# Performance work log

Hardware: AMD Instinct MI355X
Metric: run time of the kernel (lower is better)

The kernel has to match this reference:

```python
import jax, jax.numpy as jnp
import numpy as np

BS, NS, S = 4, 16384, 8
C_PLANE, RES = 64, 128
IN_DIM = 3 * C_PLANE  # 192


def _bilerp(plane, uv):
    """plane: [B,C,H,W]; uv: [B,n,2] in [0,1] -> [B,n,C] bilinear samples (border clamp)."""
    B, C, H, W = plane.shape
    x = jnp.clip(uv[..., 0], 0.0, 1.0) * (W - 1)
    y = jnp.clip(uv[..., 1], 0.0, 1.0) * (H - 1)
    x0 = jnp.floor(x).astype(jnp.int32)
    y0 = jnp.floor(y).astype(jnp.int32)
    x1 = jnp.minimum(x0 + 1, W - 1)
    y1 = jnp.minimum(y0 + 1, H - 1)
    wx = (x - x0)[:, :, None]
    wy = (y - y0)[:, :, None]
    gat = jax.vmap(lambda p, yy, xx: p[:, yy, xx].T)  # per-batch gather -> [n,C]
    f00 = gat(plane, y0, x0)
    f01 = gat(plane, y0, x1)
    f10 = gat(plane, y1, x0)
    f11 = gat(plane, y1, x1)
    return (f00 * (1 - wx) * (1 - wy) + f01 * wx * (1 - wy)
            + f10 * (1 - wx) * wy + f11 * wx * wy)


def _sample_triplane(p, feat_xz, feat_xy, feat_yz):
    """p: [B,n,3] -> concat of bilinear samples from the three planes: [B,n,3C]."""
    f_xz = _bilerp(feat_xz, p[..., jnp.array([0, 2])])
    f_xy = _bilerp(feat_xy, p[..., jnp.array([0, 1])])
    f_yz = _bilerp(feat_yz, p[..., jnp.array([1, 2])])
    return jnp.concatenate([f_xz, f_xy, f_yz], axis=-1)


def setup_inputs() -> dict:
    key = jax.random.key(0)
    ks = jax.random.split(key, 12)
    w = 0.05  # small init so predicted offsets stay near the query point
    return {
        "query_pos": jax.random.uniform(ks[0], (BS, NS, 3), dtype=jnp.float32),
        "feat_xz": jax.random.normal(ks[1], (BS, C_PLANE, RES, RES), dtype=jnp.float32),
        "feat_xy": jax.random.normal(ks[2], (BS, C_PLANE, RES, RES), dtype=jnp.float32),
        "feat_yz": jax.random.normal(ks[3], (BS, C_PLANE, RES, RES), dtype=jnp.float32),
        "W_v": jax.random.normal(ks[4], (IN_DIM, IN_DIM), dtype=jnp.float32) * w,
        "b_v": jnp.zeros((IN_DIM,), jnp.float32),
        "W_out": jax.random.normal(ks[5], (IN_DIM, IN_DIM), dtype=jnp.float32) * w,
        "b_out": jnp.zeros((IN_DIM,), jnp.float32),
        "W_off": jax.random.normal(ks[6], (3 * S, IN_DIM), dtype=jnp.float32) * w,
        "b_off": jnp.zeros((3 * S,), jnp.float32),
        "W_wt": jax.random.normal(ks[7], (S, IN_DIM), dtype=jnp.float32) * w,
        "b_wt": jnp.zeros((S,), jnp.float32),
    }


def reference(query_pos, feat_xz, feat_xy, feat_yz, W_v, b_v, W_out, b_out,
              W_off, b_off, W_wt, b_wt):
    bs, ns, _ = query_pos.shape
    # feature at query points: [bs, ns, IN_DIM]
    feature = _sample_triplane(query_pos, feat_xz, feat_xy, feat_yz)
    # predicted per-sample offsets and weights
    off = (feature @ W_off.T + b_off).reshape(bs, ns, S, 3)
    wt = (feature @ W_wt.T + b_wt)[..., None]            # [bs, ns, S, 1]
    pts = off + query_pos[:, :, None, :]                  # [bs, ns, S, 3]
    # gather features at offset locations: [bs, ns*S, IN_DIM]
    aux = _sample_triplane(pts.reshape(bs, ns * S, 3), feat_xz, feat_xy, feat_yz)
    v = (aux @ W_v.T + b_v).reshape(bs, ns, S, -1)        # [bs, ns, S, hidden]
    out = (v * wt).sum(axis=-2)                           # weighted sum over samples
    out = out @ W_out.T + b_out + feature                 # residual add
    return out  # [bs, ns, IN_DIM]
```

## Files before the change

kernel.cpp:

```cpp
#include <hip/hip_runtime.h>

#define BS 4
#define NS 16384
#define S_SAMP 8
#define CPL 64
#define RES 128
#define IN_DIM 192
#define NPTS (BS * NS)
#define PL_STRIDE (RES * RES * CPL)
#define PLANES_T_FLOATS (BS * 3 * PL_STRIDE)

__global__ __launch_bounds__(256) void transpose_planes(
    const float* __restrict__ xz, const float* __restrict__ xy,
    const float* __restrict__ yz, float* __restrict__ T) {
  __shared__ float tile[64][33];
  int blk = blockIdx.x;
  int xt = blk & 3;
  int y  = (blk >> 2) & 127;
  int pl = (blk >> 9) % 3;
  int b  = blk / 1536;
  const float* src = (pl == 0) ? xz : ((pl == 1) ? xy : yz);
  src += (size_t)b * CPL * RES * RES + (size_t)y * RES + xt * 32;
  int tid = threadIdx.x;
  int xl = tid & 31, c0 = tid >> 5;
#pragma unroll
  for (int r = 0; r < 8; ++r) {
    int c = c0 + (r << 3);
    tile[c][xl] = src[(size_t)c * RES * RES + xl];
  }
  __syncthreads();
  float* dst = T + ((size_t)(b * 3 + pl) * RES * RES + (size_t)y * RES + xt * 32) * CPL;
  int c2 = tid & 63, x0 = tid >> 6;
#pragma unroll
  for (int r = 0; r < 8; ++r) {
    int xl2 = x0 + (r << 2);
    dst[(size_t)xl2 * CPL + c2] = tile[c2][xl2];
  }
}

__global__ __launch_bounds__(192) void precompute_wc(
    const float* __restrict__ W_v, const float* __restrict__ b_v,
    const float* __restrict__ W_out, float* __restrict__ WcT,
    float* __restrict__ bc) {
  int j = blockIdx.x;
  int k = threadIdx.x;
  if (j < IN_DIM) {
    float acc = 0.f;
    for (int m = 0; m < IN_DIM; ++m)
      acc += W_out[j * IN_DIM + m] * W_v[m * IN_DIM + k];
    WcT[k * IN_DIM + j] = acc;
  } else {
    float acc = 0.f;
    for (int m = 0; m < IN_DIM; ++m)
      acc += W_out[k * IN_DIM + m] * b_v[m];
    bc[k] = acc;
  }
}

__device__ __forceinline__ void mkaddr(const float* __restrict__ pb, float u,
                                       float v, const float*& b00, int& dx,
                                       int& dy, float& wx, float& wy) {
  u = fminf(fmaxf(u, 0.f), 1.f) * 127.f;
  v = fminf(fmaxf(v, 0.f), 1.f) * 127.f;
  float xf = floorf(u), yf = floorf(v);
  wx = u - xf;
  wy = v - yf;
  int x0 = __builtin_amdgcn_readfirstlane((int)xf);
  int y0 = __builtin_amdgcn_readfirstlane((int)yf);
  dx = (x0 < 127) ? CPL : 0;
  dy = (y0 < 127) ? RES * CPL : 0;
  b00 = pb + (((y0 << 7) + x0) << 6);
}

__global__ __launch_bounds__(256, 4) void fused_sample(
    const float* __restrict__ qpos, const float* __restrict__ planesT,
    const float* __restrict__ W_off, const float* __restrict__ b_off,
    const float* __restrict__ W_wt, const float* __restrict__ b_wt,
    float* __restrict__ waux, float* __restrict__ swtg,
    float* __restrict__ featg) {
  __shared__ float feat_lds[8][IN_DIM];
  __shared__ float offwt[8][32];
  int w = threadIdx.x >> 6, lane = threadIdx.x & 63;
  int p0 = blockIdx.x * 8 + w * 2;
  int p1 = p0 + 1;
  int b0 = p0 >> 14, b1 = p1 >> 14;
  float qx0 = qpos[p0 * 3 + 0], qy0 = qpos[p0 * 3 + 1], qz0 = qpos[p0 * 3 + 2];
  float qx1 = qpos[p1 * 3 + 0], qy1 = qpos[p1 * 3 + 1], qz1 = qpos[p1 * 3 + 2];
  const float* Tb0 = planesT + (size_t)b0 * 3 * PL_STRIDE;
  const float* Tb1 = planesT + (size_t)b1 * 3 * PL_STRIDE;

  float f[6];
  {
    const float* B[6]; int DX[6], DY[6]; float WX[6], WY[6];
    mkaddr(Tb0,                 qx0, qz0, B[0], DX[0], DY[0], WX[0], WY[0]);
    mkaddr(Tb0 + PL_STRIDE,     qx0, qy0, B[1], DX[1], DY[1], WX[1], WY[1]);
    mkaddr(Tb0 + 2 * PL_STRIDE, qy0, qz0, B[2], DX[2], DY[2], WX[2], WY[2]);
    mkaddr(Tb1,                 qx1, qz1, B[3], DX[3], DY[3], WX[3], WY[3]);
    mkaddr(Tb1 + PL_STRIDE,     qx1, qy1, B[4], DX[4], DY[4], WX[4], WY[4]);
    mkaddr(Tb1 + 2 * PL_STRIDE, qy1, qz1, B[5], DX[5], DY[5], WX[5], WY[5]);
    float t00[6], t01[6], t10[6], t11[6];
#pragma unroll
    for (int i = 0; i < 6; ++i) {
      t00[i] = B[i][lane];
      t01[i] = B[i][DX[i] + lane];
      t10[i] = B[i][DY[i] + lane];
      t11[i] = B[i][DY[i] + DX[i] + lane];
    }
#pragma unroll
    for (int i = 0; i < 6; ++i) {
      float a = t00[i] + WX[i] * (t01[i] - t00[i]);
      float c = t10[i] + WX[i] * (t11[i] - t10[i]);
      f[i] = a + WY[i] * (c - a);
    }
  }
  feat_lds[w * 2 + 0][lane] = f[0];
  feat_lds[w * 2 + 0][64 + lane] = f[1];
  feat_lds[w * 2 + 0][128 + lane] = f[2];
  feat_lds[w * 2 + 1][lane] = f[3];
  feat_lds[w * 2 + 1][64 + lane] = f[4];
  feat_lds[w * 2 + 1][128 + lane] = f[5];
  __syncthreads();

  {
    int pt = lane >> 5, oj = lane & 31;
    const float* row = (oj < 24) ? (W_off + oj * IN_DIM)
                                 : (W_wt + (oj - 24) * IN_DIM);
    float bias = (oj < 24) ? b_off[oj] : b_wt[oj - 24];
    const float4* r4 = (const float4*)row;
    const float4* fl = (const float4*)feat_lds[w * 2 + pt];
    float a0 = 0.f, a1 = 0.f, a2 = 0.f, a3 = 0.f;
#pragma unroll
    for (int k4 = 0; k4 < IN_DIM / 4; ++k4) {
      float4 rv = r4[k4];
      float4 fv = fl[k4];
      a0 += rv.x * fv.x;
      a1 += rv.y * fv.y;
      a2 += rv.z * fv.z;
      a3 += rv.w * fv.w;
    }
    offwt[w * 2 + pt][oj] = bias + ((a0 + a1) + (a2 + a3));
  }
  __syncthreads();

  float wa[2][3] = {};
  float swt0 = 0.f, swt1 = 0.f;
#pragma unroll 2
  for (int s = 0; s < S_SAMP; ++s) {
    float ox0 = offwt[w * 2 + 0][3 * s + 0];
    float oy0 = offwt[w * 2 + 0][3 * s + 1];
    float oz0 = offwt[w * 2 + 0][3 * s + 2];
    float wt0 = offwt[w * 2 + 0][24 + s];
    float ox1 = offwt[w * 2 + 1][3 * s + 0];
    float oy1 = offwt[w * 2 + 1][3 * s + 1];
    float oz1 = offwt[w * 2 + 1][3 * s + 2];
    float wt1 = offwt[w * 2 + 1][24 + s];
    float px0 = qx0 + ox0, py0 = qy0 + oy0, pz0 = qz0 + oz0;
    float px1 = qx1 + ox1, py1 = qy1 + oy1, pz1 = qz1 + oz1;

    const float* B[6]; int DX[6], DY[6]; float WX[6], WY[6];
    mkaddr(Tb0,                 px0, pz0, B[0], DX[0], DY[0], WX[0], WY[0]);
    mkaddr(Tb0 + PL_STRIDE,     px0, py0, B[1], DX[1], DY[1], WX[1], WY[1]);
    mkaddr(Tb0 + 2 * PL_STRIDE, py0, pz0, B[2], DX[2], DY[2], WX[2], WY[2]);
    mkaddr(Tb1,                 px1, pz1, B[3], DX[3], DY[3], WX[3], WY[3]);
    mkaddr(Tb1 + PL_STRIDE,     px1, py1, B[4], DX[4], DY[4], WX[4], WY[4]);
    mkaddr(Tb1 + 2 * PL_STRIDE, py1, pz1, B[5], DX[5], DY[5], WX[5], WY[5]);
    float t00[6], t01[6], t10[6], t11[6];
#pragma unroll
    for (int i = 0; i < 6; ++i) {
      t00[i] = B[i][lane];
      t01[i] = B[i][DX[i] + lane];
      t10[i] = B[i][DY[i] + lane];
      t11[i] = B[i][DY[i] + DX[i] + lane];
    }
    float r[6];
#pragma unroll
    for (int i = 0; i < 6; ++i) {
      float a = t00[i] + WX[i] * (t01[i] - t00[i]);
      float c = t10[i] + WX[i] * (t11[i] - t10[i]);
      r[i] = a + WY[i] * (c - a);
    }
    wa[0][0] += wt0 * r[0]; wa[0][1] += wt0 * r[1]; wa[0][2] += wt0 * r[2];
    wa[1][0] += wt1 * r[3]; wa[1][1] += wt1 * r[4]; wa[1][2] += wt1 * r[5];
    swt0 += wt0; swt1 += wt1;
  }

  size_t o0 = (size_t)p0 * IN_DIM + lane;
  size_t o1 = (size_t)p1 * IN_DIM + lane;
  waux[o0] = wa[0][0]; waux[o0 + 64] = wa[0][1]; waux[o0 + 128] = wa[0][2];
  waux[o1] = wa[1][0]; waux[o1 + 64] = wa[1][1]; waux[o1 + 128] = wa[1][2];
  if (lane == 0) { swtg[p0] = swt0; swtg[p1] = swt1; }
  featg[o0] = f[0]; featg[o0 + 64] = f[1]; featg[o0 + 128] = f[2];
  featg[o1] = f[3]; featg[o1 + 64] = f[4]; featg[o1 + 128] = f[5];
}

__global__ __launch_bounds__(256) void out_gemm(
    const float* __restrict__ waux, const float* __restrict__ swtg,
    const float* __restrict__ WcT, const float* __restrict__ bc,
    const float* __restrict__ b_out, float* __restrict__ out) {
  __shared__ float at[64 * IN_DIM];
  int tid = threadIdx.x;
  int w = tid >> 6, lane = tid & 63;
  int p0 = blockIdx.x * 64;

  const float4* src = (const float4*)(waux + (size_t)p0 * IN_DIM);
  float4* dst4 = (float4*)at;
#pragma unroll
  for (int i = 0; i < 12; ++i) dst4[tid + i * 256] = src[tid + i * 256];
  __syncthreads();

  int pw = w * 16;
  float acc[16][3] = {};
  for (int c = 0; c < 3; ++c) {
    const float* wc = WcT + c * 64 * IN_DIM;
#pragma unroll 2
    for (int k4 = 0; k4 < 16; ++k4) {
      float v0[4], v1[4], v2[4];
#pragma unroll
      for (int kk = 0; kk < 4; ++kk) {
        const float* r = wc + (k4 * 4 + kk) * IN_DIM;
        v0[kk] = r[lane];
        v1[kk] = r[64 + lane];
        v2[kk] = r[128 + lane];
      }
#pragma unroll
      for (int q = 0; q < 16; ++q) {
        float4 a4 = *(const float4*)&at[(pw + q) * IN_DIM + c * 64 + k4 * 4];
        acc[q][0] += v0[0] * a4.x + v0[1] * a4.y + v0[2] * a4.z + v0[3] * a4.w;
        acc[q][1] += v1[0] * a4.x + v1[1] * a4.y + v1[2] * a4.z + v1[3] * a4.w;
        acc[q][2] += v2[0] * a4.x + v2[1] * a4.y + v2[2] * a4.z + v2[3] * a4.w;
      }
    }
  }

  float bcv[3], bov[3];
#pragma unroll
  for (int t = 0; t < 3; ++t) {
    bcv[t] = bc[lane + t * 64];
    bov[t] = b_out[lane + t * 64];
  }
#pragma unroll
  for (int q = 0; q < 16; ++q) {
    int p = p0 + pw + q;
    float sw = swtg[p];
#pragma unroll
    for (int t = 0; t < 3; ++t) {
      size_t o = (size_t)p * IN_DIM + lane + t * 64;
      out[o] = acc[q][t] + sw * bcv[t] + bov[t] + out[o];
    }
  }
}

extern "C" void kernel_launch(void* const* d_in, const int* in_sizes, int n_in,
                              void* d_out, int out_size, void* d_ws,
                              size_t ws_size, hipStream_t stream) {
  const float* qpos  = (const float*)d_in[0];
  const float* xz    = (const float*)d_in[1];
  const float* xy    = (const float*)d_in[2];
  const float* yz    = (const float*)d_in[3];
  const float* W_v   = (const float*)d_in[4];
  const float* b_v   = (const float*)d_in[5];
  const float* W_out = (const float*)d_in[6];
  const float* b_out = (const float*)d_in[7];
  const float* W_off = (const float*)d_in[8];
  const float* b_off = (const float*)d_in[9];
  const float* W_wt  = (const float*)d_in[10];
  const float* b_wt  = (const float*)d_in[11];

  float* ws      = (float*)d_ws;
  float* planesT = ws;
  float* waux    = planesT + PLANES_T_FLOATS;
  float* swtg    = waux + (size_t)NPTS * IN_DIM;
  float* WcT     = swtg + NPTS;
  float* bc      = WcT + IN_DIM * IN_DIM;
  float* out     = (float*)d_out;

  hipLaunchKernelGGL(transpose_planes, dim3(BS * 3 * RES * 4), dim3(256), 0,
                     stream, xz, xy, yz, planesT);
  hipLaunchKernelGGL(precompute_wc, dim3(IN_DIM + 1), dim3(IN_DIM), 0, stream,
                     W_v, b_v, W_out, WcT, bc);
  hipLaunchKernelGGL(fused_sample, dim3(NPTS / 8), dim3(256), 0, stream, qpos,
                     planesT, W_off, b_off, W_wt, b_wt, waux, swtg, out);
  hipLaunchKernelGGL(out_gemm, dim3(NPTS / 64), dim3(256), 0, stream, waux,
                     swtg, WcT, bc, b_out, out);
}
```

Before: 482.2 us.

## Software-pipeline sample tap loads and shrink out_gemm tile to 32 points

The sample loop in fused_sample now uses double-buffered tap registers, issuing the gathers for sample s+1 before interpolating sample s so memory latency overlaps arithmetic. out_gemm processes 32 points per block instead of 64, with a single flattened k loop and batched LDS reads, which halves LDS use and doubles the grid. Holding two tap sets raises register pressure and may reduce occupancy. The smaller GEMM tile reloads the weights from global memory twice as often.

```diff
diff --git a/kernel.cpp b/kernel.cpp
--- a/kernel.cpp
+++ b/kernel.cpp
@@ -72,6 +72,55 @@
   b00 = pb + (((y0 << 7) + x0) << 6);
 }
 
+struct Taps {
+  float t00[6], t01[6], t10[6], t11[6];
+  float wx[6], wy[6];
+  float wt0, wt1;
+};
+
+__device__ __forceinline__ void load_taps(
+    int s, const float* __restrict__ ow0, const float* __restrict__ ow1,
+    float qx0, float qy0, float qz0, float qx1, float qy1, float qz1,
+    const float* __restrict__ Tb0, const float* __restrict__ Tb1, int lane,
+    Taps& T) {
+  float px0 = qx0 + ow0[3 * s + 0];
+  float py0 = qy0 + ow0[3 * s + 1];
+  float pz0 = qz0 + ow0[3 * s + 2];
+  T.wt0 = ow0[24 + s];
+  float px1 = qx1 + ow1[3 * s + 0];
+  float py1 = qy1 + ow1[3 * s + 1];
+  float pz1 = qz1 + ow1[3 * s + 2];
+  T.wt1 = ow1[24 + s];
+  const float* B[6];
+  int DX[6], DY[6];
+  mkaddr(Tb0,                 px0, pz0, B[0], DX[0], DY[0], T.wx[0], T.wy[0]);
+  mkaddr(Tb0 + PL_STRIDE,     px0, py0, B[1], DX[1], DY[1], T.wx[1], T.wy[1]);
+  mkaddr(Tb0 + 2 * PL_STRIDE, py0, pz0, B[2], DX[2], DY[2], T.wx[2], T.wy[2]);
+  mkaddr(Tb1,                 px1, pz1, B[3], DX[3], DY[3], T.wx[3], T.wy[3]);
+  mkaddr(Tb1 + PL_STRIDE,     px1, py1, B[4], DX[4], DY[4], T.wx[4], T.wy[4]);
+  mkaddr(Tb1 + 2 * PL_STRIDE, py1, pz1, B[5], DX[5], DY[5], T.wx[5], T.wy[5]);
+#pragma unroll
+  for (int i = 0; i < 6; ++i) {
+    T.t00[i] = B[i][lane];
+    T.t01[i] = B[i][DX[i] + lane];
+    T.t10[i] = B[i][DY[i] + lane];
+    T.t11[i] = B[i][DY[i] + DX[i] + lane];
+  }
+}
+
+__device__ __forceinline__ void lerp_acc(const Taps& T, float wa[6],
+                                         float& swt0, float& swt1) {
+#pragma unroll
+  for (int i = 0; i < 6; ++i) {
+    float a = T.t00[i] + T.wx[i] * (T.t01[i] - T.t00[i]);
+    float c = T.t10[i] + T.wx[i] * (T.t11[i] - T.t10[i]);
+    float r = a + T.wy[i] * (c - a);
+    wa[i] += ((i < 3) ? T.wt0 : T.wt1) * r;
+  }
+  swt0 += T.wt0;
+  swt1 += T.wt1;
+}
+
 __global__ __launch_bounds__(256, 4) void fused_sample(
     const float* __restrict__ qpos, const float* __restrict__ planesT,
     const float* __restrict__ W_off, const float* __restrict__ b_off,
@@ -81,7 +130,8 @@
   __shared__ float feat_lds[8][IN_DIM];
   __shared__ float offwt[8][32];
   int w = threadIdx.x >> 6, lane = threadIdx.x & 63;
-  int p0 = blockIdx.x * 8 + w * 2;
+  int w2 = w * 2;
+  int p0 = blockIdx.x * 8 + w2;
   int p1 = p0 + 1;
   int b0 = p0 >> 14, b1 = p1 >> 14;
   float qx0 = qpos[p0 * 3 + 0], qy0 = qpos[p0 * 3 + 1], qz0 = qpos[p0 * 3 + 2];
@@ -113,12 +163,12 @@
       f[i] = a + WY[i] * (c - a);
     }
   }
-  feat_lds[w * 2 + 0][lane] = f[0];
-  feat_lds[w * 2 + 0][64 + lane] = f[1];
-  feat_lds[w * 2 + 0][128 + lane] = f[2];
-  feat_lds[w * 2 + 1][lane] = f[3];
-  feat_lds[w * 2 + 1][64 + lane] = f[4];
-  feat_lds[w * 2 + 1][128 + lane] = f[5];
+  feat_lds[w2 + 0][lane] = f[0];
+  feat_lds[w2 + 0][64 + lane] = f[1];
+  feat_lds[w2 + 0][128 + lane] = f[2];
+  feat_lds[w2 + 1][lane] = f[3];
+  feat_lds[w2 + 1][64 + lane] = f[4];
+  feat_lds[w2 + 1][128 + lane] = f[5];
   __syncthreads();
 
   {
@@ -127,7 +177,7 @@
                                  : (W_wt + (oj - 24) * IN_DIM);
     float bias = (oj < 24) ? b_off[oj] : b_wt[oj - 24];
     const float4* r4 = (const float4*)row;
-    const float4* fl = (const float4*)feat_lds[w * 2 + pt];
+    const float4* fl = (const float4*)feat_lds[w2 + pt];
     float a0 = 0.f, a1 = 0.f, a2 = 0.f, a3 = 0.f;
 #pragma unroll
     for (int k4 = 0; k4 < IN_DIM / 4; ++k4) {
@@ -138,56 +188,30 @@
       a2 += rv.z * fv.z;
       a3 += rv.w * fv.w;
     }
-    offwt[w * 2 + pt][oj] = bias + ((a0 + a1) + (a2 + a3));
+    offwt[w2 + pt][oj] = bias + ((a0 + a1) + (a2 + a3));
   }
   __syncthreads();
 
-  float wa[2][3] = {};
+  const float* ow0 = offwt[w2 + 0];
+  const float* ow1 = offwt[w2 + 1];
+  float wa[6] = {};
   float swt0 = 0.f, swt1 = 0.f;
-#pragma unroll 2
-  for (int s = 0; s < S_SAMP; ++s) {
-    float ox0 = offwt[w * 2 + 0][3 * s + 0];
-    float oy0 = offwt[w * 2 + 0][3 * s + 1];
-    float oz0 = offwt[w * 2 + 0][3 * s + 2];
-    float wt0 = offwt[w * 2 + 0][24 + s];
-    float ox1 = offwt[w * 2 + 1][3 * s + 0];
-    float oy1 = offwt[w * 2 + 1][3 * s + 1];
-    float oz1 = offwt[w * 2 + 1][3 * s + 2];
-    float wt1 = offwt[w * 2 + 1][24 + s];
-    float px0 = qx0 + ox0, py0 = qy0 + oy0, pz0 = qz0 + oz0;
-    float px1 = qx1 + ox1, py1 = qy1 + oy1, pz1 = qz1 + oz1;
-
-    const float* B[6]; int DX[6], DY[6]; float WX[6], WY[6];
-    mkaddr(Tb0,                 px0, pz0, B[0], DX[0], DY[0], WX[0], WY[0]);
-    mkaddr(Tb0 + PL_STRIDE,     px0, py0, B[1], DX[1], DY[1], WX[1], WY[1]);
-    mkaddr(Tb0 + 2 * PL_STRIDE, py0, pz0, B[2], DX[2], DY[2], WX[2], WY[2]);
-    mkaddr(Tb1,                 px1, pz1, B[3], DX[3], DY[3], WX[3], WY[3]);
-    mkaddr(Tb1 + PL_STRIDE,     px1, py1, B[4], DX[4], DY[4], WX[4], WY[4]);
-    mkaddr(Tb1 + 2 * PL_STRIDE, py1, pz1, B[5], DX[5], DY[5], WX[5], WY[5]);
-    float t00[6], t01[6], t10[6], t11[6];
-#pragma unroll
-    for (int i = 0; i < 6; ++i) {
-      t00[i] = B[i][lane];
-      t01[i] = B[i][DX[i] + lane];
-      t10[i] = B[i][DY[i] + lane];
-      t11[i] = B[i][DY[i] + DX[i] + lane];
-    }
-    float r[6];
-#pragma unroll
-    for (int i = 0; i < 6; ++i) {
-      float a = t00[i] + WX[i] * (t01[i] - t00[i]);
-      float c = t10[i] + WX[i] * (t11[i] - t10[i]);
-      r[i] = a + WY[i] * (c - a);
-    }
-    wa[0][0] += wt0 * r[0]; wa[0][1] += wt0 * r[1]; wa[0][2] += wt0 * r[2];
-    wa[1][0] += wt1 * r[3]; wa[1][1] += wt1 * r[4]; wa[1][2] += wt1 * r[5];
-    swt0 += wt0; swt1 += wt1;
+  Taps TA, TB;
+  load_taps(0, ow0, ow1, qx0, qy0, qz0, qx1, qy1, qz1, Tb0, Tb1, lane, TA);
+#pragma unroll
+  for (int s = 0; s < S_SAMP; s += 2) {
+    if (s + 1 < S_SAMP)
+      load_taps(s + 1, ow0, ow1, qx0, qy0, qz0, qx1, qy1, qz1, Tb0, Tb1, lane, TB);
+    lerp_acc(TA, wa, swt0, swt1);
+    if (s + 2 < S_SAMP)
+      load_taps(s + 2, ow0, ow1, qx0, qy0, qz0, qx1, qy1, qz1, Tb0, Tb1, lane, TA);
+    lerp_acc(TB, wa, swt0, swt1);
   }
 
   size_t o0 = (size_t)p0 * IN_DIM + lane;
   size_t o1 = (size_t)p1 * IN_DIM + lane;
-  waux[o0] = wa[0][0]; waux[o0 + 64] = wa[0][1]; waux[o0 + 128] = wa[0][2];
-  waux[o1] = wa[1][0]; waux[o1 + 64] = wa[1][1]; waux[o1 + 128] = wa[1][2];
+  waux[o0] = wa[0]; waux[o0 + 64] = wa[1]; waux[o0 + 128] = wa[2];
+  waux[o1] = wa[3]; waux[o1 + 64] = wa[4]; waux[o1 + 128] = wa[5];
   if (lane == 0) { swtg[p0] = swt0; swtg[p1] = swt1; }
   featg[o0] = f[0]; featg[o0 + 64] = f[1]; featg[o0 + 128] = f[2];
   featg[o1] = f[3]; featg[o1 + 64] = f[4]; featg[o1 + 128] = f[5];
@@ -197,38 +221,38 @@
     const float* __restrict__ waux, const float* __restrict__ swtg,
     const float* __restrict__ WcT, const float* __restrict__ bc,
     const float* __restrict__ b_out, float* __restrict__ out) {
-  __shared__ float at[64 * IN_DIM];
+  __shared__ float at[32 * IN_DIM];
   int tid = threadIdx.x;
   int w = tid >> 6, lane = tid & 63;
-  int p0 = blockIdx.x * 64;
+  int p0 = blockIdx.x * 32;
 
   const float4* src = (const float4*)(waux + (size_t)p0 * IN_DIM);
   float4* dst4 = (float4*)at;
 #pragma unroll
-  for (int i = 0; i < 12; ++i) dst4[tid + i * 256] = src[tid + i * 256];
+  for (int i = 0; i < 6; ++i) dst4[tid + i * 256] = src[tid + i * 256];
   __syncthreads();
 
-  int pw = w * 16;
-  float acc[16][3] = {};
-  for (int c = 0; c < 3; ++c) {
-    const float* wc = WcT + c * 64 * IN_DIM;
+  int pw = w * 8;
+  float acc[8][3] = {};
 #pragma unroll 2
-    for (int k4 = 0; k4 < 16; ++k4) {
-      float v0[4], v1[4], v2[4];
-#pragma unroll
-      for (int kk = 0; kk < 4; ++kk) {
-        const float* r = wc + (k4 * 4 + kk) * IN_DIM;
-        v0[kk] = r[lane];
-        v1[kk] = r[64 + lane];
-        v2[kk] = r[128 + lane];
-      }
-#pragma unroll
-      for (int q = 0; q < 16; ++q) {
-        float4 a4 = *(const float4*)&at[(pw + q) * IN_DIM + c * 64 + k4 * 4];
-        acc[q][0] += v0[0] * a4.x + v0[1] * a4.y + v0[2] * a4.z + v0[3] * a4.w;
-        acc[q][1] += v1[0] * a4.x + v1[1] * a4.y + v1[2] * a4.z + v1[3] * a4.w;
-        acc[q][2] += v2[0] * a4.x + v2[1] * a4.y + v2[2] * a4.z + v2[3] * a4.w;
-      }
+  for (int k4 = 0; k4 < 48; ++k4) {
+    float v0[4], v1[4], v2[4];
+#pragma unroll
+    for (int kk = 0; kk < 4; ++kk) {
+      const float* r = WcT + (k4 * 4 + kk) * IN_DIM;
+      v0[kk] = r[lane];
+      v1[kk] = r[64 + lane];
+      v2[kk] = r[128 + lane];
+    }
+    float4 a[8];
+#pragma unroll
+    for (int q = 0; q < 8; ++q)
+      a[q] = *(const float4*)&at[(pw + q) * IN_DIM + k4 * 4];
+#pragma unroll
+    for (int q = 0; q < 8; ++q) {
+      acc[q][0] += v0[0] * a[q].x + v0[1] * a[q].y + v0[2] * a[q].z + v0[3] * a[q].w;
+      acc[q][1] += v1[0] * a[q].x + v1[1] * a[q].y + v1[2] * a[q].z + v1[3] * a[q].w;
+      acc[q][2] += v2[0] * a[q].x + v2[1] * a[q].y + v2[2] * a[q].z + v2[3] * a[q].w;
     }
   }
 
@@ -239,7 +263,7 @@
     bov[t] = b_out[lane + t * 64];
   }
 #pragma unroll
-  for (int q = 0; q < 16; ++q) {
+  for (int q = 0; q < 8; ++q) {
     int p = p0 + pw + q;
     float sw = swtg[p];
 #pragma unroll
@@ -280,6 +304,6 @@
                      W_v, b_v, W_out, WcT, bc);
   hipLaunchKernelGGL(fused_sample, dim3(NPTS / 8), dim3(256), 0, stream, qpos,
                      planesT, W_off, b_off, W_wt, b_wt, waux, swtg, out);
-  hipLaunchKernelGGL(out_gemm, dim3(NPTS / 64), dim3(256), 0, stream, waux,
+  hipLaunchKernelGGL(out_gemm, dim3(NPTS / 32), dim3(256), 0, stream, waux,
                      swtg, WcT, bc, b_out, out);
 }
```

Result: faster. 470.1 us (-2.5%).
